# Kernel optimization log

Hardware: AMD Instinct MI355X
Metric: run time of the kernel (lower is better)

The kernel has to match this reference:

```python
import jax, jax.numpy as jnp
import numpy as np

N_HEAD = 8
ALPHA = 5.0
EPS = 1e-12  # matches F.normalize default


def setup_inputs() -> dict:
    key = jax.random.key(0)
    kq, kk, kv = jax.random.split(key, 3)
    B, D, T = 4, 1024, 2048
    q = jax.random.normal(kq, (B, D, T), dtype=jnp.float32)
    k = jax.random.normal(kk, (B, D, T), dtype=jnp.float32)
    v = jax.random.normal(kv, (B, D, T), dtype=jnp.float32)
    return {"q": q, "k": k, "v": v}


def _l2norm(x, axis):
    n = jnp.sqrt(jnp.sum(x * x, axis=axis, keepdims=True))
    return x / jnp.maximum(n, EPS)


def reference(q, k, v):
    B, D, Tq = q.shape
    Tk = k.shape[-1]
    Dv = v.shape[-2]
    h = N_HEAD
    d = D // h
    dv = Dv // h
    qh = q.reshape(B, h, d, Tq)
    kh = k.reshape(B, h, d, Tk)
    vh = v.reshape(B, h, dv, Tk)
    # cosine-normalize over per-head channel dim (axis -2)
    qn = _l2norm(qh, axis=-2)
    kn = _l2norm(kh, axis=-2)
    qk = ALPHA * jnp.einsum('bhdq,bhdk->bhqk', qn, kn)
    sm = jax.nn.softmax(qk, axis=-1)
    # (sm.unsqueeze(-3) * v.unsqueeze(-2)).sum(-1)  ==  einsum over k
    out = jnp.einsum('bhqk,bhdk->bhdq', sm, vh)
    return out.reshape(B, Dv, Tq)
```

## Files before the change

kernel.cpp:

```cpp
#include <hip/hip_runtime.h>


#define T_SEQ 2048
#define DH 128
#define BH 32

typedef float f32x4 __attribute__((ext_vector_type(4)));
typedef __bf16 bf16x8 __attribute__((ext_vector_type(8)));
typedef __bf16 bf16x4 __attribute__((ext_vector_type(4)));

__device__ __forceinline__ void async_copy16(const void* g, void* l) {
  __builtin_amdgcn_global_load_lds(
      (const __attribute__((address_space(1))) void*)g,
      (__attribute__((address_space(3))) void*)l, 16, 0, 0);
}

__global__ __launch_bounds__(256) void norm_transpose_kernel(
    const float* __restrict__ src, __bf16* __restrict__ dst, float scale) {
  __shared__ float tile[64 * 133];
  __shared__ float part[4][64];
  __shared__ float inv_t[64];
  const int bh = blockIdx.x >> 5;
  const int t0 = (blockIdx.x & 31) * 64;
  const int tid = threadIdx.x;

#pragma unroll
  for (int it = 0; it < 8; ++it) {
    int c = it * 256 + tid;
    int ch = c >> 4;
    int t4 = (c & 15) * 4;
    f32x4 v = *(const f32x4*)(src + (size_t)(bh * DH + ch) * T_SEQ + t0 + t4);
#pragma unroll
    for (int i = 0; i < 4; ++i) tile[(t4 + i) * 133 + ch] = v[i];
  }
  __syncthreads();
  const int t = tid & 63;
  const int seg = tid >> 6;
  float ss = 0.f;
#pragma unroll
  for (int i = 0; i < 8; ++i) {
    f32x4 x = *(const f32x4*)(tile + t * 133 + seg * 32 + i * 4);
    ss += x[0]*x[0] + x[1]*x[1] + x[2]*x[2] + x[3]*x[3];
  }
  part[seg][t] = ss;
  __syncthreads();
  if (tid < 64) {
    float n = sqrtf(part[0][tid] + part[1][tid] + part[2][tid] + part[3][tid]);
    inv_t[tid] = scale / fmaxf(n, 1e-12f);
  }
  __syncthreads();
  const int t_o = tid >> 2;
  const int c0 = (tid & 3) * 32;
  const float inv = inv_t[t_o];
  __bf16* drow = dst + (size_t)(bh * T_SEQ + t0 + t_o) * DH + c0;
#pragma unroll
  for (int cc = 0; cc < 4; ++cc) {
    f32x4 a = *(const f32x4*)(tile + t_o * 133 + c0 + cc * 8);
    f32x4 b = *(const f32x4*)(tile + t_o * 133 + c0 + cc * 8 + 4);
    bf16x8 ob;
    ob[0] = (__bf16)(a[0]*inv); ob[1] = (__bf16)(a[1]*inv);
    ob[2] = (__bf16)(a[2]*inv); ob[3] = (__bf16)(a[3]*inv);
    ob[4] = (__bf16)(b[0]*inv); ob[5] = (__bf16)(b[1]*inv);
    ob[6] = (__bf16)(b[2]*inv); ob[7] = (__bf16)(b[3]*inv);
    *(bf16x8*)(drow + cc * 8) = ob;
  }
}

__global__ __launch_bounds__(256) void cast_bf16_kernel(
    const float* __restrict__ src, __bf16* __restrict__ dst, int n8) {
  int i = blockIdx.x * 256 + threadIdx.x;
  if (i >= n8) return;
  f32x4 a = *(const f32x4*)(src + (size_t)i * 8);
  f32x4 b = *(const f32x4*)(src + (size_t)i * 8 + 4);
  bf16x8 ob;
  ob[0] = (__bf16)a[0]; ob[1] = (__bf16)a[1]; ob[2] = (__bf16)a[2]; ob[3] = (__bf16)a[3];
  ob[4] = (__bf16)b[0]; ob[5] = (__bf16)b[1]; ob[6] = (__bf16)b[2]; ob[7] = (__bf16)b[3];
  *(bf16x8*)(dst + (size_t)i * 8) = ob;
}

__global__ __launch_bounds__(256, 2) void attn_kernel(
    const __bf16* __restrict__ qn, const __bf16* __restrict__ kn,
    const __bf16* __restrict__ vb, float* __restrict__ out) {
  __shared__ __bf16 lds_k[16 * 512];
  __shared__ __bf16 lds_v[16 * 512];
  __shared__ __bf16 p_buf[8 * 16 * 68];

  const int bh = blockIdx.x >> 4;
  const int q0 = (blockIdx.x & 15) * 128;
  const int tid = threadIdx.x;
  const int w = tid >> 6;
  const int lane = tid & 63;
  const int qi = lane & 15;
  const int g = lane >> 4;

  const __bf16* kbase = kn + (size_t)bh * (T_SEQ * DH);
  const __bf16* vbase = vb + (size_t)bh * (DH * T_SEQ);

  bf16x8 qf[2][4];
#pragma unroll
  for (int nt = 0; nt < 2; ++nt) {
    const __bf16* qrow =
        qn + (size_t)(bh * T_SEQ + q0 + w * 32 + nt * 16 + qi) * DH + g * 8;
#pragma unroll
    for (int s = 0; s < 4; ++s) qf[nt][s] = *(const bf16x8*)(qrow + s * 32);
  }

  f32x4 o_acc[2][8];
#pragma unroll
  for (int nt = 0; nt < 2; ++nt)
#pragma unroll
    for (int i = 0; i < 8; ++i) o_acc[nt][i] = (f32x4)(0.f);
  float m_run[2] = {-__builtin_inff(), -__builtin_inff()};
  float l_run[2] = {0.f, 0.f};

  for (int k0 = 0; k0 < T_SEQ; k0 += 64) {
#pragma unroll
    for (int i = 0; i < 8; ++i) {
      const int I = w * 8 + i;
      if (I < 16) {
        const int mt = I >> 2, s = I & 3;
        const __bf16* ga =
            kbase + (size_t)(k0 + mt * 16 + qi) * DH + s * 32 + g * 8;
        async_copy16(ga, lds_k + I * 512);
      } else {
        const int f = I - 16;
        const int mt = f >> 1, st = f & 1;
        const __bf16* ga =
            vbase + (size_t)(mt * 16 + qi) * T_SEQ + k0 + st * 32 + g * 8;
        async_copy16(ga, lds_v + f * 512);
      }
    }
    __syncthreads();

    f32x4 sacc[2][4];
#pragma unroll
    for (int nt = 0; nt < 2; ++nt)
#pragma unroll
      for (int mt = 0; mt < 4; ++mt) sacc[nt][mt] = (f32x4)(0.f);
#pragma unroll
    for (int s = 0; s < 4; ++s) {
#pragma unroll
      for (int mt = 0; mt < 4; ++mt) {
        bf16x8 a = *(const bf16x8*)(lds_k + ((mt * 4 + s) * 64 + lane) * 8);
        sacc[0][mt] = __builtin_amdgcn_mfma_f32_16x16x32_bf16(a, qf[0][s], sacc[0][mt], 0, 0, 0);
        sacc[1][mt] = __builtin_amdgcn_mfma_f32_16x16x32_bf16(a, qf[1][s], sacc[1][mt], 0, 0, 0);
      }
    }

#pragma unroll
    for (int nt = 0; nt < 2; ++nt) {
      float tmax = -__builtin_inff();
#pragma unroll
      for (int mt = 0; mt < 4; ++mt)
#pragma unroll
        for (int r = 0; r < 4; ++r) tmax = fmaxf(tmax, sacc[nt][mt][r]);
      tmax = fmaxf(tmax, __shfl_xor(tmax, 16, 64));
      tmax = fmaxf(tmax, __shfl_xor(tmax, 32, 64));
      const float m_new = fmaxf(m_run[nt], tmax);
      const float corr = __expf(m_run[nt] - m_new);

      __bf16* pw = p_buf + (size_t)((w * 2 + nt) * 16 + qi) * 68;
      float rsum = 0.f;
#pragma unroll
      for (int mt = 0; mt < 4; ++mt) {
        bf16x4 pb;
#pragma unroll
        for (int r = 0; r < 4; ++r) {
          float e = __expf(sacc[nt][mt][r] - m_new);
          rsum += e;
          pb[r] = (__bf16)e;
        }
        *(bf16x4*)(pw + mt * 16 + g * 4) = pb;
      }
      rsum += __shfl_xor(rsum, 16, 64);
      rsum += __shfl_xor(rsum, 32, 64);
      l_run[nt] = l_run[nt] * corr + rsum;
      m_run[nt] = m_new;
#pragma unroll
      for (int i = 0; i < 8; ++i) {
        o_acc[nt][i][0] *= corr; o_acc[nt][i][1] *= corr;
        o_acc[nt][i][2] *= corr; o_acc[nt][i][3] *= corr;
      }
    }

#pragma unroll
    for (int st = 0; st < 2; ++st) {
      bf16x8 pf0 = *(const bf16x8*)(p_buf + (size_t)((w * 2 + 0) * 16 + qi) * 68 + st * 32 + g * 8);
      bf16x8 pf1 = *(const bf16x8*)(p_buf + (size_t)((w * 2 + 1) * 16 + qi) * 68 + st * 32 + g * 8);
#pragma unroll
      for (int mt = 0; mt < 8; ++mt) {
        bf16x8 a = *(const bf16x8*)(lds_v + ((mt * 2 + st) * 64 + lane) * 8);
        o_acc[0][mt] = __builtin_amdgcn_mfma_f32_16x16x32_bf16(a, pf0, o_acc[0][mt], 0, 0, 0);
        o_acc[1][mt] = __builtin_amdgcn_mfma_f32_16x16x32_bf16(a, pf1, o_acc[1][mt], 0, 0, 0);
      }
    }
    __syncthreads();
  }

#pragma unroll
  for (int nt = 0; nt < 2; ++nt) {
    const float rinv = 1.f / l_run[nt];
    const int tq = q0 + w * 32 + nt * 16 + qi;
#pragma unroll
    for (int mt = 0; mt < 8; ++mt) {
#pragma unroll
      for (int r = 0; r < 4; ++r) {
        int ch = mt * 16 + g * 4 + r;
        out[(size_t)(bh * DH + ch) * T_SEQ + tq] = o_acc[nt][mt][r] * rinv;
      }
    }
  }
}

extern "C" void kernel_launch(void* const* d_in, const int* in_sizes, int n_in,
                              void* d_out, int out_size, void* d_ws, size_t ws_size,
                              hipStream_t stream) {
  const float* q = (const float*)d_in[0];
  const float* k = (const float*)d_in[1];
  const float* v = (const float*)d_in[2];
  float* out = (float*)d_out;
  const size_t n = (size_t)BH * T_SEQ * DH;
  if (ws_size < 3 * n * sizeof(__bf16)) return;
  __bf16* qn = (__bf16*)d_ws;
  __bf16* kn = qn + n;
  __bf16* vbf = kn + n;

  norm_transpose_kernel<<<dim3(BH * 32), dim3(256), 0, stream>>>(q, qn, 5.0f);
  norm_transpose_kernel<<<dim3(BH * 32), dim3(256), 0, stream>>>(k, kn, 1.0f);
  cast_bf16_kernel<<<dim3((int)(n / 8 / 256)), dim3(256), 0, stream>>>(v, vbf, (int)(n / 8));
  attn_kernel<<<dim3(512), dim3(256), 0, stream>>>(qn, kn, vbf, out);
}
```

Measured before the change: 241.5 us.

## Fuse prepasses, double-buffer K/V tiles, drop online-softmax max tracking

Merges the K normalize-transpose and the V cast into one prepass launch. Q normalization moves into the attention kernel's prologue, so the qn workspace round trip goes away. The attention loop now double-buffers K/V in LDS so the next tile loads while the current one computes, and it uses an XOR swizzle for the P buffer. It also drops the running max and rescaling, because scores are bounded by |ALPHA|=5 after cosine normalization, so a plain exp stays stable.

```diff
diff --git a/kernel.cpp b/kernel.cpp
--- a/kernel.cpp
+++ b/kernel.cpp
@@ -15,21 +15,33 @@
       (__attribute__((address_space(3))) void*)l, 16, 0, 0);
 }
 
-__global__ __launch_bounds__(256) void norm_transpose_kernel(
-    const float* __restrict__ src, __bf16* __restrict__ dst, float scale) {
+__global__ __launch_bounds__(256) void prepass_kernel(
+    const float* __restrict__ ksrc, const float* __restrict__ vsrc,
+    __bf16* __restrict__ kn, __bf16* __restrict__ vb) {
   __shared__ float tile[64 * 133];
   __shared__ float part[4][64];
   __shared__ float inv_t[64];
+  const int tid = threadIdx.x;
+
+  if (blockIdx.x >= 1024) {
+    int i = (blockIdx.x - 1024) * 256 + tid;
+    f32x4 a = *(const f32x4*)(vsrc + (size_t)i * 8);
+    f32x4 b = *(const f32x4*)(vsrc + (size_t)i * 8 + 4);
+    bf16x8 ob;
+    ob[0] = (__bf16)a[0]; ob[1] = (__bf16)a[1]; ob[2] = (__bf16)a[2]; ob[3] = (__bf16)a[3];
+    ob[4] = (__bf16)b[0]; ob[5] = (__bf16)b[1]; ob[6] = (__bf16)b[2]; ob[7] = (__bf16)b[3];
+    *(bf16x8*)(vb + (size_t)i * 8) = ob;
+    return;
+  }
+
   const int bh = blockIdx.x >> 5;
   const int t0 = (blockIdx.x & 31) * 64;
-  const int tid = threadIdx.x;
-
 #pragma unroll
   for (int it = 0; it < 8; ++it) {
     int c = it * 256 + tid;
     int ch = c >> 4;
     int t4 = (c & 15) * 4;
-    f32x4 v = *(const f32x4*)(src + (size_t)(bh * DH + ch) * T_SEQ + t0 + t4);
+    f32x4 v = *(const f32x4*)(ksrc + (size_t)(bh * DH + ch) * T_SEQ + t0 + t4);
 #pragma unroll
     for (int i = 0; i < 4; ++i) tile[(t4 + i) * 133 + ch] = v[i];
   }
@@ -46,13 +58,13 @@
   __syncthreads();
   if (tid < 64) {
     float n = sqrtf(part[0][tid] + part[1][tid] + part[2][tid] + part[3][tid]);
-    inv_t[tid] = scale / fmaxf(n, 1e-12f);
+    inv_t[tid] = 1.f / fmaxf(n, 1e-12f);
   }
   __syncthreads();
   const int t_o = tid >> 2;
   const int c0 = (tid & 3) * 32;
   const float inv = inv_t[t_o];
-  __bf16* drow = dst + (size_t)(bh * T_SEQ + t0 + t_o) * DH + c0;
+  __bf16* drow = kn + (size_t)(bh * T_SEQ + t0 + t_o) * DH + c0;
 #pragma unroll
   for (int cc = 0; cc < 4; ++cc) {
     f32x4 a = *(const f32x4*)(tile + t_o * 133 + c0 + cc * 8);
@@ -66,43 +78,68 @@
   }
 }
 
-__global__ __launch_bounds__(256) void cast_bf16_kernel(
-    const float* __restrict__ src, __bf16* __restrict__ dst, int n8) {
-  int i = blockIdx.x * 256 + threadIdx.x;
-  if (i >= n8) return;
-  f32x4 a = *(const f32x4*)(src + (size_t)i * 8);
-  f32x4 b = *(const f32x4*)(src + (size_t)i * 8 + 4);
-  bf16x8 ob;
-  ob[0] = (__bf16)a[0]; ob[1] = (__bf16)a[1]; ob[2] = (__bf16)a[2]; ob[3] = (__bf16)a[3];
-  ob[4] = (__bf16)b[0]; ob[5] = (__bf16)b[1]; ob[6] = (__bf16)b[2]; ob[7] = (__bf16)b[3];
-  *(bf16x8*)(dst + (size_t)i * 8) = ob;
+__device__ __forceinline__ void stage_tiles(
+    const __bf16* kbase, const __bf16* vbase, __bf16* lk, __bf16* lv,
+    int koff, int w, int qi, int g) {
+#pragma unroll
+  for (int i = 0; i < 4; ++i) {
+    const int f = w * 4 + i;
+    const int mt = f >> 2, s = f & 3;
+    async_copy16(kbase + (size_t)(koff + mt * 16 + qi) * DH + s * 32 + g * 8,
+                 lk + f * 512);
+  }
+#pragma unroll
+  for (int i = 0; i < 4; ++i) {
+    const int f = w * 4 + i;
+    const int mt = f >> 1, st = f & 1;
+    async_copy16(vbase + (size_t)(mt * 16 + qi) * T_SEQ + koff + st * 32 + g * 8,
+                 lv + f * 512);
+  }
 }
 
 __global__ __launch_bounds__(256, 2) void attn_kernel(
-    const __bf16* __restrict__ qn, const __bf16* __restrict__ kn,
+    const float* __restrict__ q, const __bf16* __restrict__ kn,
     const __bf16* __restrict__ vb, float* __restrict__ out) {
-  __shared__ __bf16 lds_k[16 * 512];
-  __shared__ __bf16 lds_v[16 * 512];
-  __shared__ __bf16 p_buf[8 * 16 * 68];
+  __shared__ __align__(16) __bf16 lds_k[2][16 * 512];
+  __shared__ __align__(16) __bf16 lds_v[2][16 * 512];
+  __shared__ __align__(16) __bf16 p_buf[8 * 1024];
 
   const int bh = blockIdx.x >> 4;
   const int q0 = (blockIdx.x & 15) * 128;
   const int tid = threadIdx.x;
-  const int w = tid >> 6;
-  const int lane = tid & 63;
-  const int qi = lane & 15;
-  const int g = lane >> 4;
+  const int w = tid >> 6, lane = tid & 63;
+  const int qi = lane & 15, g = lane >> 4;
 
   const __bf16* kbase = kn + (size_t)bh * (T_SEQ * DH);
   const __bf16* vbase = vb + (size_t)bh * (DH * T_SEQ);
+  const float* qsrc = q + (size_t)bh * (DH * T_SEQ);
+
+  stage_tiles(kbase, vbase, lds_k[0], lds_v[0], 0, w, qi, g);
 
   bf16x8 qf[2][4];
 #pragma unroll
   for (int nt = 0; nt < 2; ++nt) {
-    const __bf16* qrow =
-        qn + (size_t)(bh * T_SEQ + q0 + w * 32 + nt * 16 + qi) * DH + g * 8;
-#pragma unroll
-    for (int s = 0; s < 4; ++s) qf[nt][s] = *(const bf16x8*)(qrow + s * 32);
+    const int t = q0 + w * 32 + nt * 16 + qi;
+    float xv[32];
+    float ss = 0.f;
+#pragma unroll
+    for (int s = 0; s < 4; ++s)
+#pragma unroll
+      for (int j = 0; j < 8; ++j) {
+        float x = qsrc[(size_t)(s * 32 + g * 8 + j) * T_SEQ + t];
+        xv[s * 8 + j] = x;
+        ss += x * x;
+      }
+    ss += __shfl_xor(ss, 16, 64);
+    ss += __shfl_xor(ss, 32, 64);
+    const float inv = 5.0f / fmaxf(sqrtf(ss), 1e-12f);
+#pragma unroll
+    for (int s = 0; s < 4; ++s) {
+      bf16x8 f;
+#pragma unroll
+      for (int j = 0; j < 8; ++j) f[j] = (__bf16)(xv[s * 8 + j] * inv);
+      qf[nt][s] = f;
+    }
   }
 
   f32x4 o_acc[2][8];
@@ -110,105 +147,79 @@
   for (int nt = 0; nt < 2; ++nt)
 #pragma unroll
     for (int i = 0; i < 8; ++i) o_acc[nt][i] = (f32x4)(0.f);
-  float m_run[2] = {-__builtin_inff(), -__builtin_inff()};
-  float l_run[2] = {0.f, 0.f};
-
-  for (int k0 = 0; k0 < T_SEQ; k0 += 64) {
-#pragma unroll
-    for (int i = 0; i < 8; ++i) {
-      const int I = w * 8 + i;
-      if (I < 16) {
-        const int mt = I >> 2, s = I & 3;
-        const __bf16* ga =
-            kbase + (size_t)(k0 + mt * 16 + qi) * DH + s * 32 + g * 8;
-        async_copy16(ga, lds_k + I * 512);
-      } else {
-        const int f = I - 16;
-        const int mt = f >> 1, st = f & 1;
-        const __bf16* ga =
-            vbase + (size_t)(mt * 16 + qi) * T_SEQ + k0 + st * 32 + g * 8;
-        async_copy16(ga, lds_v + f * 512);
-      }
-    }
+  float lsum[2] = {0.f, 0.f};
+
+  const int swz = (qi & 7) << 3;
+  __bf16* pw0 = p_buf + (w * 2 + 0) * 1024 + qi * 64;
+  __bf16* pw1 = p_buf + (w * 2 + 1) * 1024 + qi * 64;
+
+  for (int it = 0; it < 32; ++it) {
     __syncthreads();
-
+    const int cur = it & 1;
+    if (it + 1 < 32)
+      stage_tiles(kbase, vbase, lds_k[cur ^ 1], lds_v[cur ^ 1],
+                  (it + 1) * 64, w, qi, g);
+
+    const __bf16* lk = lds_k[cur];
     f32x4 sacc[2][4];
 #pragma unroll
     for (int nt = 0; nt < 2; ++nt)
 #pragma unroll
       for (int mt = 0; mt < 4; ++mt) sacc[nt][mt] = (f32x4)(0.f);
 #pragma unroll
-    for (int s = 0; s < 4; ++s) {
+    for (int s = 0; s < 4; ++s)
 #pragma unroll
       for (int mt = 0; mt < 4; ++mt) {
-        bf16x8 a = *(const bf16x8*)(lds_k + ((mt * 4 + s) * 64 + lane) * 8);
+        bf16x8 a = *(const bf16x8*)(lk + ((mt * 4 + s) * 64 + lane) * 8);
         sacc[0][mt] = __builtin_amdgcn_mfma_f32_16x16x32_bf16(a, qf[0][s], sacc[0][mt], 0, 0, 0);
         sacc[1][mt] = __builtin_amdgcn_mfma_f32_16x16x32_bf16(a, qf[1][s], sacc[1][mt], 0, 0, 0);
       }
-    }
 
 #pragma unroll
     for (int nt = 0; nt < 2; ++nt) {
-      float tmax = -__builtin_inff();
-#pragma unroll
-      for (int mt = 0; mt < 4; ++mt)
-#pragma unroll
-        for (int r = 0; r < 4; ++r) tmax = fmaxf(tmax, sacc[nt][mt][r]);
-      tmax = fmaxf(tmax, __shfl_xor(tmax, 16, 64));
-      tmax = fmaxf(tmax, __shfl_xor(tmax, 32, 64));
-      const float m_new = fmaxf(m_run[nt], tmax);
-      const float corr = __expf(m_run[nt] - m_new);
-
-      __bf16* pw = p_buf + (size_t)((w * 2 + nt) * 16 + qi) * 68;
-      float rsum = 0.f;
+      __bf16* pw = nt ? pw1 : pw0;
+      float rs = 0.f;
 #pragma unroll
       for (int mt = 0; mt < 4; ++mt) {
         bf16x4 pb;
 #pragma unroll
         for (int r = 0; r < 4; ++r) {
-          float e = __expf(sacc[nt][mt][r] - m_new);
-          rsum += e;
+          float e = __expf(sacc[nt][mt][r]);
+          rs += e;
           pb[r] = (__bf16)e;
         }
-        *(bf16x4*)(pw + mt * 16 + g * 4) = pb;
-      }
-      rsum += __shfl_xor(rsum, 16, 64);
-      rsum += __shfl_xor(rsum, 32, 64);
-      l_run[nt] = l_run[nt] * corr + rsum;
-      m_run[nt] = m_new;
-#pragma unroll
-      for (int i = 0; i < 8; ++i) {
-        o_acc[nt][i][0] *= corr; o_acc[nt][i][1] *= corr;
-        o_acc[nt][i][2] *= corr; o_acc[nt][i][3] *= corr;
-      }
+        *(bf16x4*)(pw + ((mt * 16 + g * 4) ^ swz)) = pb;
+      }
+      lsum[nt] += rs;
     }
 
+    const __bf16* lv = lds_v[cur];
 #pragma unroll
     for (int st = 0; st < 2; ++st) {
-      bf16x8 pf0 = *(const bf16x8*)(p_buf + (size_t)((w * 2 + 0) * 16 + qi) * 68 + st * 32 + g * 8);
-      bf16x8 pf1 = *(const bf16x8*)(p_buf + (size_t)((w * 2 + 1) * 16 + qi) * 68 + st * 32 + g * 8);
+      bf16x8 pf0 = *(const bf16x8*)(pw0 + ((st * 32 + g * 8) ^ swz));
+      bf16x8 pf1 = *(const bf16x8*)(pw1 + ((st * 32 + g * 8) ^ swz));
 #pragma unroll
       for (int mt = 0; mt < 8; ++mt) {
-        bf16x8 a = *(const bf16x8*)(lds_v + ((mt * 2 + st) * 64 + lane) * 8);
+        bf16x8 a = *(const bf16x8*)(lv + ((mt * 2 + st) * 64 + lane) * 8);
         o_acc[0][mt] = __builtin_amdgcn_mfma_f32_16x16x32_bf16(a, pf0, o_acc[0][mt], 0, 0, 0);
         o_acc[1][mt] = __builtin_amdgcn_mfma_f32_16x16x32_bf16(a, pf1, o_acc[1][mt], 0, 0, 0);
       }
     }
-    __syncthreads();
   }
 
 #pragma unroll
   for (int nt = 0; nt < 2; ++nt) {
-    const float rinv = 1.f / l_run[nt];
+    float l = lsum[nt];
+    l += __shfl_xor(l, 16, 64);
+    l += __shfl_xor(l, 32, 64);
+    const float rinv = 1.f / l;
     const int tq = q0 + w * 32 + nt * 16 + qi;
 #pragma unroll
-    for (int mt = 0; mt < 8; ++mt) {
-#pragma unroll
-      for (int r = 0; r < 4; ++r) {
-        int ch = mt * 16 + g * 4 + r;
-        out[(size_t)(bh * DH + ch) * T_SEQ + tq] = o_acc[nt][mt][r] * rinv;
-      }
-    }
+    for (int mt = 0; mt < 8; ++mt)
+#pragma unroll
+      for (int r = 0; r < 4; ++r)
+        out[(size_t)(bh * DH + mt * 16 + g * 4 + r) * T_SEQ + tq] =
+            o_acc[nt][mt][r] * rinv;
   }
 }
 
@@ -220,13 +231,10 @@
   const float* v = (const float*)d_in[2];
   float* out = (float*)d_out;
   const size_t n = (size_t)BH * T_SEQ * DH;
-  if (ws_size < 3 * n * sizeof(__bf16)) return;
-  __bf16* qn = (__bf16*)d_ws;
-  __bf16* kn = qn + n;
+  if (ws_size < 2 * n * sizeof(__bf16)) return;
+  __bf16* kn = (__bf16*)d_ws;
   __bf16* vbf = kn + n;
 
-  norm_transpose_kernel<<<dim3(BH * 32), dim3(256), 0, stream>>>(q, qn, 5.0f);
-  norm_transpose_kernel<<<dim3(BH * 32), dim3(256), 0, stream>>>(k, kn, 1.0f);
-  cast_bf16_kernel<<<dim3((int)(n / 8 / 256)), dim3(256), 0, stream>>>(v, vbf, (int)(n / 8));
-  attn_kernel<<<dim3(512), dim3(256), 0, stream>>>(qn, kn, vbf, out);
-}
+  prepass_kernel<<<dim3(1024 + 4096), dim3(256), 0, stream>>>(k, v, kn, vbf);
+  attn_kernel<<<dim3(512), dim3(256), 0, stream>>>(q, kn, vbf, out);
+}
```

Result: faster. 214.7 us (-11.1%).
